# Kernel optimization log

Measured on AMD Instinct MI355X. Metric: run time of the kernel, lower is better.

The kernel has to match this reference:

```python
import jax, jax.numpy as jnp
import numpy as np

KY = KX = 7
PAD_Y = (KY - 1) // 2
PAD_X = (KX - 1) // 2
SIGMA_COLOR = 0.1
SIGMA_SPACE = (1.5, 1.5)


def _gaussian1d(ksize, sigma):
    x = jnp.arange(ksize, dtype=jnp.float32) - float(ksize // 2)
    g = jnp.exp(-jnp.square(x) / (2.0 * sigma * sigma))
    return g / jnp.sum(g)


def setup_inputs() -> dict:
    key = jax.random.key(0)
    x = jax.random.uniform(key, (8, 3, 512, 512), dtype=jnp.float32)
    return {"input": x}


def reference(input) -> jnp.ndarray:
    B, C, H, W = input.shape
    padded = jnp.pad(input, ((0, 0), (0, 0), (PAD_Y, PAD_Y), (PAD_X, PAD_X)), mode="reflect")
    # patches[b,c,h,w,k] = padded[b,c,h+i,w+j], k = i*KX + j  (ky-major, matches torch unfold)
    patches = jnp.stack(
        [padded[:, :, i:i + H, j:j + W] for i in range(KY) for j in range(KX)],
        axis=-1,
    )  # (B, C, H, W, KY*KX)
    diff = patches - input[..., None]
    # l1 color distance, squared: (sum_c |diff|)^2 -> (B,1,H,W,K)
    color_dist_sq = jnp.square(jnp.sum(jnp.abs(diff), axis=1, keepdims=True))
    color_kernel = jnp.exp((-0.5 / (SIGMA_COLOR ** 2)) * color_dist_sq)
    ky1d = _gaussian1d(KY, SIGMA_SPACE[0])
    kx1d = _gaussian1d(KX, SIGMA_SPACE[1])
    space_kernel = (ky1d[:, None] * kx1d[None, :]).reshape(1, 1, 1, 1, KY * KX)
    kernel = space_kernel * color_kernel  # (B,1,H,W,K)
    out = jnp.sum(patches * kernel, axis=-1) / jnp.sum(kernel, axis=-1)
    return out
```

## Files before the change

kernel.cpp:

```cpp
#include <hip/hip_runtime.h>

#define HH 512
#define WW 512
#define CH 3
#define NTX 64
#define NTY 4
#define PX  2
#define SPAN (NTX * PX)
#define TILE_W  (SPAN + 6)
#define TILE_H  (NTY + 6)
#define PHYS_W  138

#define K1f (-72.13475204444817f)
#define K2f (-0.3205988979753252f)

__device__ __forceinline__ int reflect_idx(int v, int n) {
    v = (v < 0) ? -v : v;
    return (v >= n) ? (2 * (n - 1) - v) : v;
}

__device__ __forceinline__ float fast_exp2(float x) {
#if __has_builtin(__builtin_amdgcn_exp2f)
    return __builtin_amdgcn_exp2f(x);
#else
    return exp2f(x);
#endif
}

__device__ __forceinline__ int phys(int c) { return c + (c >> 5); }

__global__ __launch_bounds__(NTX * NTY)
void bilateral_kernel(const float* __restrict__ in, float* __restrict__ out) {
    __shared__ float sm[CH * TILE_H * PHYS_W];

    const int bx0 = blockIdx.x * SPAN;
    const int by0 = blockIdx.y * NTY;
    const int b   = blockIdx.z;
    const float* inb = in + (size_t)b * CH * HH * WW;

    for (int c = 0; c < CH; ++c) {
        for (int ty = threadIdx.y; ty < TILE_H; ty += NTY) {
            const int gy = reflect_idx(by0 + ty - 3, HH);
            const float* grow = inb + (c * HH + gy) * WW;
            float* srow = &sm[(c * TILE_H + ty) * PHYS_W];
            for (int tx = threadIdx.x; tx < TILE_W; tx += NTX) {
                const int gx = reflect_idx(bx0 + tx - 3, WW);
                srow[phys(tx)] = grow[gx];
            }
        }
    }
    __syncthreads();

    const int lx = threadIdx.x;
    const int ty = threadIdx.y;
    const int cb = PX * lx;

    int pcol[8];
#pragma unroll
    for (int k = 0; k < 8; ++k) pcol[k] = phys(cb + k);

    const float* smb = sm + ty * PHYS_W;

    float c0[PX], c1[PX], c2[PX];
#pragma unroll
    for (int p = 0; p < PX; ++p) {
        c0[p] = smb[(0 * TILE_H + 3) * PHYS_W + pcol[3 + p]];
        c1[p] = smb[(1 * TILE_H + 3) * PHYS_W + pcol[3 + p]];
        c2[p] = smb[(2 * TILE_H + 3) * PHYS_W + pcol[3 + p]];
    }

    float n0[PX] = {0, 0}, n1[PX] = {0, 0}, n2[PX] = {0, 0}, den[PX] = {0, 0};

#pragma unroll
    for (int i = 0; i < 7; ++i) {
        float A0[8], A1[8], A2[8];
#pragma unroll
        for (int k = 0; k < 8; ++k) {
            A0[k] = smb[(0 * TILE_H + i) * PHYS_W + pcol[k]];
            A1[k] = smb[(1 * TILE_H + i) * PHYS_W + pcol[k]];
            A2[k] = smb[(2 * TILE_H + i) * PHYS_W + pcol[k]];
        }

#pragma unroll
        for (int j = 0; j < 7; ++j) {
#pragma unroll
            for (int p = 0; p < PX; ++p) {
                const float v0 = A0[j + p];
                const float v1 = A1[j + p];
                const float v2 = A2[j + p];
                const float d  = fabsf(v0 - c0[p]) + fabsf(v1 - c1[p]) + fabsf(v2 - c2[p]);
                const float lnw = (float)((i - 3) * (i - 3) + (j - 3) * (j - 3)) * K2f;
                const float w  = fast_exp2(fmaf(d * K1f, d, lnw));
                n0[p]  = fmaf(w, v0, n0[p]);
                n1[p]  = fmaf(w, v1, n1[p]);
                n2[p]  = fmaf(w, v2, n2[p]);
                den[p] += w;
            }
        }
    }

    const int y  = by0 + ty;
    const int x0 = bx0 + cb;
    float* outb = out + (size_t)b * CH * HH * WW;

    float inv[PX];
#pragma unroll
    for (int p = 0; p < PX; ++p) inv[p] = 1.0f / den[p];

    float2 o;
    o.x = n0[0] * inv[0]; o.y = n0[1] * inv[1];
    *reinterpret_cast<float2*>(&outb[(0 * HH + y) * WW + x0]) = o;
    o.x = n1[0] * inv[0]; o.y = n1[1] * inv[1];
    *reinterpret_cast<float2*>(&outb[(1 * HH + y) * WW + x0]) = o;
    o.x = n2[0] * inv[0]; o.y = n2[1] * inv[1];
    *reinterpret_cast<float2*>(&outb[(2 * HH + y) * WW + x0]) = o;
}

extern "C" void kernel_launch(void* const* d_in, const int* in_sizes, int n_in,
                              void* d_out, int out_size, void* d_ws, size_t ws_size,
                              hipStream_t stream) {
    const float* in = (const float*)d_in[0];
    float* out = (float*)d_out;
    const int B = in_sizes[0] / (CH * HH * WW);
    dim3 grid(WW / SPAN, HH / NTY, B);
    dim3 block(NTX, NTY, 1);
    bilateral_kernel<<<grid, block, 0, stream>>>(in, out);
}
```

Before: 62.01 us.

## Register-block four output rows per thread to reuse shared-memory row loads

```diff
diff --git a/kernel.cpp b/kernel.cpp
--- a/kernel.cpp
+++ b/kernel.cpp
@@ -5,11 +5,13 @@
 #define CH 3
 #define NTX 64
 #define NTY 4
-#define PX  2
-#define SPAN (NTX * PX)
-#define TILE_W  (SPAN + 6)
-#define TILE_H  (NTY + 6)
-#define PHYS_W  138
+#define PXT 2
+#define PYT 4
+#define SPANX (NTX * PXT)
+#define SPANY (NTY * PYT)
+#define TILE_W (SPANX + 6)
+#define TILE_H (SPANY + 6)
+#define PHYS_W 138
 
 #define K1f (-72.13475204444817f)
 #define K2f (-0.3205988979753252f)
@@ -33,8 +35,8 @@
 void bilateral_kernel(const float* __restrict__ in, float* __restrict__ out) {
     __shared__ float sm[CH * TILE_H * PHYS_W];
 
-    const int bx0 = blockIdx.x * SPAN;
-    const int by0 = blockIdx.y * NTY;
+    const int bx0 = blockIdx.x * SPANX;
+    const int by0 = blockIdx.y * SPANY;
     const int b   = blockIdx.z;
     const float* inb = in + (size_t)b * CH * HH * WW;
 
@@ -52,68 +54,76 @@
     __syncthreads();
 
     const int lx = threadIdx.x;
-    const int ty = threadIdx.y;
-    const int cb = PX * lx;
+    const int rb = threadIdx.y * PYT;
+    const int cb = PXT * lx;
 
-    int pcol[8];
+    int vcol[8];
 #pragma unroll
-    for (int k = 0; k < 8; ++k) pcol[k] = phys(cb + k);
-
-    const float* smb = sm + ty * PHYS_W;
-
-    float c0[PX], c1[PX], c2[PX];
-#pragma unroll
-    for (int p = 0; p < PX; ++p) {
-        c0[p] = smb[(0 * TILE_H + 3) * PHYS_W + pcol[3 + p]];
-        c1[p] = smb[(1 * TILE_H + 3) * PHYS_W + pcol[3 + p]];
-        c2[p] = smb[(2 * TILE_H + 3) * PHYS_W + pcol[3 + p]];
+    for (int k = 0; k < 8; ++k) {
+        vcol[k] = rb * PHYS_W + phys(cb + k);
+        asm("" : "+v"(vcol[k]));
     }
 
-    float n0[PX] = {0, 0}, n1[PX] = {0, 0}, n2[PX] = {0, 0}, den[PX] = {0, 0};
+    float cc0[PYT][PXT], cc1[PYT][PXT], cc2[PYT][PXT];
+#pragma unroll
+    for (int py = 0; py < PYT; ++py) {
+#pragma unroll
+        for (int p = 0; p < PXT; ++p) {
+            cc0[py][p] = sm[(0 * TILE_H + py + 3) * PHYS_W + vcol[3 + p]];
+            cc1[py][p] = sm[(1 * TILE_H + py + 3) * PHYS_W + vcol[3 + p]];
+            cc2[py][p] = sm[(2 * TILE_H + py + 3) * PHYS_W + vcol[3 + p]];
+        }
+    }
+
+    float n0[PYT][PXT] = {}, n1[PYT][PXT] = {}, n2[PYT][PXT] = {}, den[PYT][PXT] = {};
 
 #pragma unroll
-    for (int i = 0; i < 7; ++i) {
+    for (int r = 0; r < PYT + 6; ++r) {
         float A0[8], A1[8], A2[8];
 #pragma unroll
         for (int k = 0; k < 8; ++k) {
-            A0[k] = smb[(0 * TILE_H + i) * PHYS_W + pcol[k]];
-            A1[k] = smb[(1 * TILE_H + i) * PHYS_W + pcol[k]];
-            A2[k] = smb[(2 * TILE_H + i) * PHYS_W + pcol[k]];
+            A0[k] = sm[(0 * TILE_H + r) * PHYS_W + vcol[k]];
+            A1[k] = sm[(1 * TILE_H + r) * PHYS_W + vcol[k]];
+            A2[k] = sm[(2 * TILE_H + r) * PHYS_W + vcol[k]];
         }
-
 #pragma unroll
-        for (int j = 0; j < 7; ++j) {
+        for (int py = 0; py < PYT; ++py) {
+            const int i = r - py;
+            if (i < 0 || i > 6) continue;
 #pragma unroll
-            for (int p = 0; p < PX; ++p) {
-                const float v0 = A0[j + p];
-                const float v1 = A1[j + p];
-                const float v2 = A2[j + p];
-                const float d  = fabsf(v0 - c0[p]) + fabsf(v1 - c1[p]) + fabsf(v2 - c2[p]);
-                const float lnw = (float)((i - 3) * (i - 3) + (j - 3) * (j - 3)) * K2f;
-                const float w  = fast_exp2(fmaf(d * K1f, d, lnw));
-                n0[p]  = fmaf(w, v0, n0[p]);
-                n1[p]  = fmaf(w, v1, n1[p]);
-                n2[p]  = fmaf(w, v2, n2[p]);
-                den[p] += w;
+            for (int j = 0; j < 7; ++j) {
+#pragma unroll
+                for (int p = 0; p < PXT; ++p) {
+                    const float v0 = A0[j + p];
+                    const float v1 = A1[j + p];
+                    const float v2 = A2[j + p];
+                    const float d  = fabsf(v0 - cc0[py][p]) + fabsf(v1 - cc1[py][p]) + fabsf(v2 - cc2[py][p]);
+                    const float lnw = (float)((i - 3) * (i - 3) + (j - 3) * (j - 3)) * K2f;
+                    const float w  = fast_exp2(fmaf(d * K1f, d, lnw));
+                    n0[py][p]  = fmaf(w, v0, n0[py][p]);
+                    n1[py][p]  = fmaf(w, v1, n1[py][p]);
+                    n2[py][p]  = fmaf(w, v2, n2[py][p]);
+                    den[py][p] += w;
+                }
             }
         }
     }
 
-    const int y  = by0 + ty;
+    float* outb = out + (size_t)b * CH * HH * WW;
     const int x0 = bx0 + cb;
-    float* outb = out + (size_t)b * CH * HH * WW;
-
-    float inv[PX];
 #pragma unroll
-    for (int p = 0; p < PX; ++p) inv[p] = 1.0f / den[p];
-
-    float2 o;
-    o.x = n0[0] * inv[0]; o.y = n0[1] * inv[1];
-    *reinterpret_cast<float2*>(&outb[(0 * HH + y) * WW + x0]) = o;
-    o.x = n1[0] * inv[0]; o.y = n1[1] * inv[1];
-    *reinterpret_cast<float2*>(&outb[(1 * HH + y) * WW + x0]) = o;
-    o.x = n2[0] * inv[0]; o.y = n2[1] * inv[1];
-    *reinterpret_cast<float2*>(&outb[(2 * HH + y) * WW + x0]) = o;
+    for (int py = 0; py < PYT; ++py) {
+        const int y = by0 + rb + py;
+        const float i0 = 1.0f / den[py][0];
+        const float i1 = 1.0f / den[py][1];
+        float2 o;
+        o.x = n0[py][0] * i0; o.y = n0[py][1] * i1;
+        *reinterpret_cast<float2*>(&outb[(0 * HH + y) * WW + x0]) = o;
+        o.x = n1[py][0] * i0; o.y = n1[py][1] * i1;
+        *reinterpret_cast<float2*>(&outb[(1 * HH + y) * WW + x0]) = o;
+        o.x = n2[py][0] * i0; o.y = n2[py][1] * i1;
+        *reinterpret_cast<float2*>(&outb[(2 * HH + y) * WW + x0]) = o;
+    }
 }
 
 extern "C" void kernel_launch(void* const* d_in, const int* in_sizes, int n_in,
@@ -122,7 +132,7 @@
     const float* in = (const float*)d_in[0];
     float* out = (float*)d_out;
     const int B = in_sizes[0] / (CH * HH * WW);
-    dim3 grid(WW / SPAN, HH / NTY, B);
+    dim3 grid(WW / SPANX, HH / SPANY, B);
     dim3 block(NTX, NTY, 1);
     bilateral_kernel<<<grid, block, 0, stream>>>(in, out);
 }
```

After: 200.6 us. +223.6%, slower.

## Switch per-thread work from horizontal pixel pairs to vertical 4-pixel columns

Applied to the files above, without the earlier changes.

```diff
diff --git a/kernel.cpp b/kernel.cpp
--- a/kernel.cpp
+++ b/kernel.cpp
@@ -5,11 +5,11 @@
 #define CH 3
 #define NTX 64
 #define NTY 4
-#define PX  2
-#define SPAN (NTX * PX)
-#define TILE_W  (SPAN + 6)
-#define TILE_H  (NTY + 6)
-#define PHYS_W  138
+#define PY  4
+#define SPANY (NTY * PY)
+#define TILE_W 70
+#define TILE_H (SPANY + 6)
+#define NELEM (CH * TILE_H * TILE_W)
 
 #define K1f (-72.13475204444817f)
 #define K2f (-0.3205988979753252f)
@@ -27,93 +27,83 @@
 #endif
 }
 
-__device__ __forceinline__ int phys(int c) { return c + (c >> 5); }
-
 __global__ __launch_bounds__(NTX * NTY)
 void bilateral_kernel(const float* __restrict__ in, float* __restrict__ out) {
-    __shared__ float sm[CH * TILE_H * PHYS_W];
+    __shared__ float sm[NELEM];
 
-    const int bx0 = blockIdx.x * SPAN;
-    const int by0 = blockIdx.y * NTY;
+    const int bx0 = blockIdx.x * NTX;
+    const int by0 = blockIdx.y * SPANY;
     const int b   = blockIdx.z;
+    const int tid = threadIdx.y * NTX + threadIdx.x;
     const float* inb = in + (size_t)b * CH * HH * WW;
 
-    for (int c = 0; c < CH; ++c) {
-        for (int ty = threadIdx.y; ty < TILE_H; ty += NTY) {
-            const int gy = reflect_idx(by0 + ty - 3, HH);
-            const float* grow = inb + (c * HH + gy) * WW;
-            float* srow = &sm[(c * TILE_H + ty) * PHYS_W];
-            for (int tx = threadIdx.x; tx < TILE_W; tx += NTX) {
-                const int gx = reflect_idx(bx0 + tx - 3, WW);
-                srow[phys(tx)] = grow[gx];
-            }
-        }
+    for (int idx = tid; idx < NELEM; idx += NTX * NTY) {
+        int c  = idx / (TILE_H * TILE_W);
+        int r  = idx - c * (TILE_H * TILE_W);
+        int ty = r / TILE_W;
+        int tx = r - ty * TILE_W;
+        const int gy = reflect_idx(by0 + ty - 3, HH);
+        const int gx = reflect_idx(bx0 + tx - 3, WW);
+        sm[idx] = inb[(c * HH + gy) * WW + gx];
     }
     __syncthreads();
 
     const int lx = threadIdx.x;
-    const int ty = threadIdx.y;
-    const int cb = PX * lx;
+    const int rb = threadIdx.y * PY;
 
-    int pcol[8];
+    const float* smb = sm + rb * TILE_W + lx;
+#define SMEM(c, r, j) smb[((c) * TILE_H + (r)) * TILE_W + (j)]
+
+    float c0[PY], c1[PY], c2[PY];
 #pragma unroll
-    for (int k = 0; k < 8; ++k) pcol[k] = phys(cb + k);
-
-    const float* smb = sm + ty * PHYS_W;
-
-    float c0[PX], c1[PX], c2[PX];
-#pragma unroll
-    for (int p = 0; p < PX; ++p) {
-        c0[p] = smb[(0 * TILE_H + 3) * PHYS_W + pcol[3 + p]];
-        c1[p] = smb[(1 * TILE_H + 3) * PHYS_W + pcol[3 + p]];
-        c2[p] = smb[(2 * TILE_H + 3) * PHYS_W + pcol[3 + p]];
+    for (int py = 0; py < PY; ++py) {
+        c0[py] = SMEM(0, py + 3, 3);
+        c1[py] = SMEM(1, py + 3, 3);
+        c2[py] = SMEM(2, py + 3, 3);
     }
 
-    float n0[PX] = {0, 0}, n1[PX] = {0, 0}, n2[PX] = {0, 0}, den[PX] = {0, 0};
+    float n0[PY] = {}, n1[PY] = {}, n2[PY] = {}, den[PY] = {};
 
 #pragma unroll
-    for (int i = 0; i < 7; ++i) {
-        float A0[8], A1[8], A2[8];
-#pragma unroll
-        for (int k = 0; k < 8; ++k) {
-            A0[k] = smb[(0 * TILE_H + i) * PHYS_W + pcol[k]];
-            A1[k] = smb[(1 * TILE_H + i) * PHYS_W + pcol[k]];
-            A2[k] = smb[(2 * TILE_H + i) * PHYS_W + pcol[k]];
-        }
-
+    for (int r = 0; r < PY + 6; ++r) {
+        float A0[7], A1[7], A2[7];
 #pragma unroll
         for (int j = 0; j < 7; ++j) {
+            A0[j] = SMEM(0, r, j);
+            A1[j] = SMEM(1, r, j);
+            A2[j] = SMEM(2, r, j);
+        }
 #pragma unroll
-            for (int p = 0; p < PX; ++p) {
-                const float v0 = A0[j + p];
-                const float v1 = A1[j + p];
-                const float v2 = A2[j + p];
-                const float d  = fabsf(v0 - c0[p]) + fabsf(v1 - c1[p]) + fabsf(v2 - c2[p]);
-                const float lnw = (float)((i - 3) * (i - 3) + (j - 3) * (j - 3)) * K2f;
-                const float w  = fast_exp2(fmaf(d * K1f, d, lnw));
-                n0[p]  = fmaf(w, v0, n0[p]);
-                n1[p]  = fmaf(w, v1, n1[p]);
-                n2[p]  = fmaf(w, v2, n2[p]);
-                den[p] += w;
+        for (int py = 0; py < PY; ++py) {
+            const int i = r - py;
+            if (i < 0 || i > 6) continue;
+#pragma unroll
+            for (int j = 0; j < 7; ++j) {
+                const float v0 = A0[j];
+                const float v1 = A1[j];
+                const float v2 = A2[j];
+                const float d  = fabsf(v0 - c0[py]) + fabsf(v1 - c1[py]) + fabsf(v2 - c2[py]);
+                const float LK = (float)((i - 3) * (i - 3) + (j - 3) * (j - 3)) * K2f;
+                const float w  = fast_exp2(fmaf(d * K1f, d, LK));
+                n0[py]  = fmaf(w, v0, n0[py]);
+                n1[py]  = fmaf(w, v1, n1[py]);
+                n2[py]  = fmaf(w, v2, n2[py]);
+                den[py] += w;
             }
         }
     }
+#undef SMEM
 
-    const int y  = by0 + ty;
-    const int x0 = bx0 + cb;
     float* outb = out + (size_t)b * CH * HH * WW;
-
-    float inv[PX];
+    const int x = bx0 + lx;
 #pragma unroll
-    for (int p = 0; p < PX; ++p) inv[p] = 1.0f / den[p];
-
-    float2 o;
-    o.x = n0[0] * inv[0]; o.y = n0[1] * inv[1];
-    *reinterpret_cast<float2*>(&outb[(0 * HH + y) * WW + x0]) = o;
-    o.x = n1[0] * inv[0]; o.y = n1[1] * inv[1];
-    *reinterpret_cast<float2*>(&outb[(1 * HH + y) * WW + x0]) = o;
-    o.x = n2[0] * inv[0]; o.y = n2[1] * inv[1];
-    *reinterpret_cast<float2*>(&outb[(2 * HH + y) * WW + x0]) = o;
+    for (int py = 0; py < PY; ++py) {
+        const int y = by0 + rb + py;
+        const float inv = 1.0f / den[py];
+        outb[(0 * HH + y) * WW + x] = n0[py] * inv;
+        outb[(1 * HH + y) * WW + x] = n1[py] * inv;
+        outb[(2 * HH + y) * WW + x] = n2[py] * inv;
+    }
 }
 
 extern "C" void kernel_launch(void* const* d_in, const int* in_sizes, int n_in,
@@ -122,7 +112,7 @@
     const float* in = (const float*)d_in[0];
     float* out = (float*)d_out;
     const int B = in_sizes[0] / (CH * HH * WW);
-    dim3 grid(WW / SPAN, HH / NTY, B);
+    dim3 grid(WW / NTX, HH / SPANY, B);
     dim3 block(NTX, NTY, 1);
     bilateral_kernel<<<grid, block, 0, stream>>>(in, out);
 }
```

After: 82.00 us. +32.2%, slower.
